# Optimization experiments

Hardware: AMD Instinct MI355X
Metric: run time of the kernel (lower is better)

## Reference

```python
import jax, jax.numpy as jnp
import numpy as np

B, LI, LJ, D = 32, 512, 512, 512
NN_DIM = 256  # agg output dim = 2*NN_DIM = 512


def setup_inputs() -> dict:
    key = jax.random.key(0)
    k1, k2, k3 = jax.random.split(key, 3)
    i = jax.random.normal(k1, (B, LI, D), dtype=jnp.float32)
    j = jax.random.normal(k2, (B, LJ, D), dtype=jnp.float32)
    W_agg = jax.random.normal(k3, (D, 2 * NN_DIM), dtype=jnp.float32) * (1.0 / np.sqrt(D))
    b_agg = jnp.zeros((2 * NN_DIM,), dtype=jnp.float32)
    return {"i": i, "j": j, "W_agg": W_agg, "b_agg": b_agg}


def _agg(x, W, b):
    # shared aggregation net: Dense(2*nn_dim) + tanh, then mean-pool over time
    # x: [B, L, D] -> [B, 2*nn_dim]
    return jnp.mean(jnp.tanh(jnp.einsum('bld,dh->blh', x, W) + b), axis=1)


def reference(i, j, W_agg, b_agg):
    # cross-attention scores: [B, Li, Lj]
    weight = jnp.einsum('bik,bjk->bij', i, j)
    # row softmax (over Lj) -> weights to aggregate j per i-position
    weight_j = jax.nn.softmax(weight, axis=2)
    # column softmax (over Li) -> weights to aggregate i per j-position
    weight_i = jax.nn.softmax(weight, axis=1)
    weighted_i = jnp.einsum('bij,bid->bjd', weight_i, i)  # [B, Lj, D]
    weighted_j = jnp.einsum('bij,bjd->bid', weight_j, j)  # [B, Li, D]
    output_i = jnp.abs(i - weighted_j)  # [B, Li, D]
    output_j = jnp.abs(j - weighted_i)  # [B, Lj, D]
    oi = _agg(output_i, W_agg, b_agg)   # [B, 2*nn_dim]
    oj = _agg(output_j, W_agg, b_agg)   # [B, 2*nn_dim]
    # K.mean(K.stack([oi, oj], axis=1), axis=1)
    return 0.5 * (oi + oj)
```

## Files before the change

kernel.cpp:

```cpp
#include <hip/hip_runtime.h>
#include <math.h>

#define B_ 32
#define L_ 512
#define D_ 512
#define H_ 512

typedef unsigned short u16;
typedef _Float16 h16;
typedef h16 half8 __attribute__((ext_vector_type(8)));
typedef float f32x4 __attribute__((ext_vector_type(4)));

#define SW(r, c) ((c) ^ (((r) >> 1) & 3))

typedef __attribute__((address_space(1))) void gvoid;
typedef __attribute__((address_space(3))) void svoid;
__device__ __forceinline__ void async_cp16(const void* g, void* l) {
    __builtin_amdgcn_global_load_lds((gvoid*)g, (svoid*)l, 16, 0, 0);
}

__device__ __forceinline__ u16 f2h(float x) {
    h16 h = (h16)x;
    u16 r;
    __builtin_memcpy(&r, &h, 2);
    return r;
}
__device__ __forceinline__ float h2f(u16 u) {
    h16 h;
    __builtin_memcpy(&h, &u, 2);
    return (float)h;
}
__device__ __forceinline__ float fast_tanh(float x) {
    return 1.0f - 2.0f / (__expf(2.0f * x) + 1.0f);
}

__device__ __forceinline__ void xcd_decode16(int n, int& z, int& tile) {
    int xcd = n & 7, w = n >> 3;
    z = xcd + 8 * (w >> 4);
    tile = w & 15;
}

__global__ __launch_bounds__(256) void cvt_all(const float* __restrict__ I,
                                               const float* __restrict__ Jm,
                                               const float* __restrict__ W,
                                               u16* __restrict__ Ih, u16* __restrict__ IhT,
                                               u16* __restrict__ Jh, u16* __restrict__ JhT,
                                               u16* __restrict__ WT,
                                               float* __restrict__ out) {
    const int z = blockIdx.z;
    const float* src;
    u16* h;
    u16* hT;
    size_t base;
    if (z < 32) {
        src = I; h = Ih; hT = IhT; base = (size_t)z * 512 * 512;
    } else if (z < 64) {
        src = Jm; h = Jh; hT = JhT; base = (size_t)(z - 32) * 512 * 512;
    } else {
        src = W; h = nullptr; hT = WT; base = 0;
        out[(blockIdx.y * 8 + blockIdx.x) * 256 + threadIdx.x] = 0.0f;
    }
    const int r0 = blockIdx.y * 64, c0 = blockIdx.x * 64;
    __shared__ u16 t[64][66];
    const int tid = threadIdx.x;
    const int tr = tid >> 4, tc4 = (tid & 15) * 4;
#pragma unroll
    for (int rep = 0; rep < 4; ++rep) {
        int r = rep * 16 + tr;
        f32x4 v = *(const f32x4*)(src + base + (size_t)(r0 + r) * 512 + c0 + tc4);
        unsigned h0 = f2h(v[0]), h1 = f2h(v[1]), h2 = f2h(v[2]), h3 = f2h(v[3]);
        if (h)
            *(uint2*)(h + base + (size_t)(r0 + r) * 512 + c0 + tc4) =
                make_uint2(h0 | (h1 << 16), h2 | (h3 << 16));
        t[r][tc4] = (u16)h0; t[r][tc4 + 1] = (u16)h1;
        t[r][tc4 + 2] = (u16)h2; t[r][tc4 + 3] = (u16)h3;
    }
    __syncthreads();
#pragma unroll
    for (int rep = 0; rep < 4; ++rep) {
        int r = rep * 16 + tr;
        unsigned a = t[tc4][r], b = t[tc4 + 1][r], c = t[tc4 + 2][r], d = t[tc4 + 3][r];
        *(uint2*)(hT + base + (size_t)(c0 + r) * 512 + r0 + tc4) =
            make_uint2(a | (b << 16), c | (d << 16));
    }
}

__global__ __launch_bounds__(256, 2) void score_mfma(const u16* __restrict__ Ih,
                                                     const u16* __restrict__ Jh,
                                                     u16* __restrict__ P_un,
                                                     u16* __restrict__ P_unT,
                                                     float* __restrict__ rtmax,
                                                     float* __restrict__ rtsum,
                                                     float* __restrict__ ctmax,
                                                     float* __restrict__ ctsum) {
    int b, tile;
    xcd_decode16(blockIdx.x, b, tile);
    const int i0 = (tile >> 2) * 128, j0 = (tile & 3) * 128;
    __shared__ u16 Ah[128 * 32], Bh[128 * 32];
    const int tid = threadIdx.x;
    const int wave = tid >> 6, lane = tid & 63;
    const int wm = (wave >> 1) * 64, wn = (wave & 1) * 64;
    const int lr = lane & 15, q = lane >> 4;
    const size_t boff = (size_t)b * L_ * D_;
    const u16* Ibh = Ih + boff;
    const u16* Jbh = Jh + boff;

    f32x4 acc[4][4] = {};

    for (int k0 = 0; k0 < D_; k0 += 32) {
#pragma unroll
        for (int h = 0; h < 2; ++h) {
            int g = wave * 2 + h;
            int r = g * 16 + (lane >> 2);
            int cg = SW(r, lane & 3);
            async_cp16(Ibh + (size_t)(i0 + r) * D_ + k0 + cg * 8, (char*)Ah + g * 1024);
            async_cp16(Jbh + (size_t)(j0 + r) * D_ + k0 + cg * 8, (char*)Bh + g * 1024);
        }
        __syncthreads();
        half8 af[4], bf[4];
#pragma unroll
        for (int mi = 0; mi < 4; ++mi) {
            int r = wm + mi * 16 + lr;
            af[mi] = *(const half8*)&Ah[r * 32 + SW(r, q) * 8];
        }
#pragma unroll
        for (int ni = 0; ni < 4; ++ni) {
            int r = wn + ni * 16 + lr;
            bf[ni] = *(const half8*)&Bh[r * 32 + SW(r, q) * 8];
        }
#pragma unroll
        for (int mi = 0; mi < 4; ++mi)
#pragma unroll
            for (int ni = 0; ni < 4; ++ni)
                acc[mi][ni] = __builtin_amdgcn_mfma_f32_16x16x32_f16(af[mi], bf[ni], acc[mi][ni], 0, 0, 0);
        __syncthreads();
    }

    float rm[4][4];
#pragma unroll
    for (int mi = 0; mi < 4; ++mi)
#pragma unroll
        for (int r4 = 0; r4 < 4; ++r4) {
            float t = fmaxf(fmaxf(acc[mi][0][r4], acc[mi][1][r4]),
                            fmaxf(acc[mi][2][r4], acc[mi][3][r4]));
#pragma unroll
            for (int off = 1; off < 16; off <<= 1) t = fmaxf(t, __shfl_xor(t, off));
            rm[mi][r4] = t;
        }
    float cm[4];
#pragma unroll
    for (int ni = 0; ni < 4; ++ni) {
        float u = -1e30f;
#pragma unroll
        for (int mi = 0; mi < 4; ++mi)
#pragma unroll
            for (int r4 = 0; r4 < 4; ++r4) u = fmaxf(u, acc[mi][ni][r4]);
        u = fmaxf(u, __shfl_xor(u, 16));
        u = fmaxf(u, __shfl_xor(u, 32));
        cm[ni] = u;
    }

    u16* Pu_b = P_un + (size_t)b * L_ * L_;
    u16* PuT_b = P_unT + (size_t)b * L_ * L_;
    float rs[4][4] = {};
    float cs[4] = {};
#pragma unroll
    for (int mi = 0; mi < 4; ++mi)
#pragma unroll
        for (int ni = 0; ni < 4; ++ni) {
            int i_base = i0 + wm + mi * 16 + q * 4;
            int j = j0 + wn + ni * 16 + lr;
            unsigned pc[4];
#pragma unroll
            for (int r4 = 0; r4 < 4; ++r4) {
                float er = __expf(acc[mi][ni][r4] - rm[mi][r4]);
                rs[mi][r4] += er;
                Pu_b[(size_t)(i_base + r4) * L_ + j] = f2h(er);
                float ec = __expf(acc[mi][ni][r4] - cm[ni]);
                cs[ni] += ec;
                pc[r4] = f2h(ec);
            }
            *(uint2*)&PuT_b[(size_t)j * L_ + i_base] =
                make_uint2(pc[0] | (pc[1] << 16), pc[2] | (pc[3] << 16));
        }

    const int gr = (j0 + wn) >> 6;
    const int gc = (i0 + wm) >> 6;
#pragma unroll
    for (int mi = 0; mi < 4; ++mi)
#pragma unroll
        for (int r4 = 0; r4 < 4; ++r4) {
            float s = rs[mi][r4];
#pragma unroll
            for (int off = 1; off < 16; off <<= 1) s += __shfl_xor(s, off);
            if (lr == 0) {
                int i = i0 + wm + mi * 16 + q * 4 + r4;
                rtmax[((size_t)b * L_ + i) * 8 + gr] = rm[mi][r4];
                rtsum[((size_t)b * L_ + i) * 8 + gr] = s;
            }
        }
#pragma unroll
    for (int ni = 0; ni < 4; ++ni) {
        float s = cs[ni];
        s += __shfl_xor(s, 16);
        s += __shfl_xor(s, 32);
        if (q == 0) {
            int j = j0 + wn + ni * 16 + lr;
            ctmax[((size_t)b * L_ + j) * 8 + gc] = cm[ni];
            ctsum[((size_t)b * L_ + j) * 8 + gc] = s;
        }
    }
}

__global__ __launch_bounds__(256, 2) void absdiff_scaled(const u16* __restrict__ P_un,
                                                         const u16* __restrict__ P_unT,
                                                         const float* __restrict__ rtmax,
                                                         const float* __restrict__ rtsum,
                                                         const float* __restrict__ ctmax,
                                                         const float* __restrict__ ctsum,
                                                         const u16* __restrict__ JhT,
                                                         const u16* __restrict__ IhT,
                                                         const u16* __restrict__ Ih,
                                                         const u16* __restrict__ Jh,
                                                         u16* __restrict__ Xall) {
    int zz, tile;
    xcd_decode16(blockIdx.x, zz, tile);
    const int side = zz >> 5, b = zz & 31;
    const int a0 = (tile >> 2) * 128, d0 = (tile & 3) * 128;
    const u16* Pb = (side ? P_unT : P_un) + (size_t)b * L_ * L_;
    const float* tmax = (side ? ctmax : rtmax) + (size_t)b * L_ * 8;
    const float* tsum = (side ? ctsum : rtsum) + (size_t)b * L_ * 8;
    const u16* Vt = (side ? IhT : JhT) + (size_t)b * D_ * L_;
    const u16* Oh = (side ? Jh : Ih) + (size_t)b * L_ * D_;
    u16* Xb = Xall + (size_t)zz * L_ * D_;

    __shared__ u16 As[128 * 32], Bs[128 * 32];
    __shared__ float sc[8][128];
    const int tid = threadIdx.x;
    const int wave = tid >> 6, lane = tid & 63;
    const int wm = (wave >> 1) * 64, wn = (wave & 1) * 64;
    const int lr = lane & 15, q = lane >> 4;

    if (tid < 128) {
        const float* tm = tmax + (size_t)(a0 + tid) * 8;
        const float* ts = tsum + (size_t)(a0 + tid) * 8;
        f32x4 m0 = *(const f32x4*)tm, m1 = *(const f32x4*)(tm + 4);
        f32x4 s0 = *(const f32x4*)ts, s1 = *(const f32x4*)(ts + 4);
        float m = fmaxf(fmaxf(fmaxf(m0[0], m0[1]), fmaxf(m0[2], m0[3])),
                        fmaxf(fmaxf(m1[0], m1[1]), fmaxf(m1[2], m1[3])));
        float e0 = __expf(m0[0] - m), e1 = __expf(m0[1] - m);
        float e2 = __expf(m0[2] - m), e3 = __expf(m0[3] - m);
        float e4 = __expf(m1[0] - m), e5 = __expf(m1[1] - m);
        float e6 = __expf(m1[2] - m), e7 = __expf(m1[3] - m);
        float inv = 1.0f / (e0 * s0[0] + e1 * s0[1] + e2 * s0[2] + e3 * s0[3] +
                            e4 * s1[0] + e5 * s1[1] + e6 * s1[2] + e7 * s1[3]);
        sc[0][tid] = e0 * inv; sc[1][tid] = e1 * inv;
        sc[2][tid] = e2 * inv; sc[3][tid] = e3 * inv;
        sc[4][tid] = e4 * inv; sc[5][tid] = e5 * inv;
        sc[6][tid] = e6 * inv; sc[7][tid] = e7 * inv;
    }
    __syncthreads();

    f32x4 acc[4][4] = {};

    for (int k0 = 0; k0 < L_; k0 += 32) {
#pragma unroll
        for (int h = 0; h < 2; ++h) {
            int g = wave * 2 + h;
            int r = g * 16 + (lane >> 2);
            int cg = SW(r, lane & 3);
            async_cp16(Pb + (size_t)(a0 + r) * L_ + k0 + cg * 8, (char*)As + g * 1024);
            async_cp16(Vt + (size_t)(d0 + r) * L_ + k0 + cg * 8, (char*)Bs + g * 1024);
        }
        __syncthreads();
        const int gk = k0 >> 6;
        half8 af[4], bf[4];
#pragma unroll
        for (int mi = 0; mi < 4; ++mi) {
            int r = wm + mi * 16 + lr;
            h16 s = (h16)sc[gk][r];
            half8 s8 = {s, s, s, s, s, s, s, s};
            af[mi] = *(const half8*)&As[r * 32 + SW(r, q) * 8] * s8;
        }
#pragma unroll
        for (int ni = 0; ni < 4; ++ni) {
            int r = wn + ni * 16 + lr;
            bf[ni] = *(const half8*)&Bs[r * 32 + SW(r, q) * 8];
        }
#pragma unroll
        for (int mi = 0; mi < 4; ++mi)
#pragma unroll
            for (int ni = 0; ni < 4; ++ni)
                acc[mi][ni] = __builtin_amdgcn_mfma_f32_16x16x32_f16(af[mi], bf[ni], acc[mi][ni], 0, 0, 0);
        __syncthreads();
    }

#pragma unroll
    for (int mi = 0; mi < 4; ++mi)
#pragma unroll
        for (int ni = 0; ni < 4; ++ni) {
            int i = a0 + wm + mi * 16 + q * 4;
            int d = d0 + wn + ni * 16 + lr;
#pragma unroll
            for (int r4 = 0; r4 < 4; ++r4) {
                float x = fabsf(h2f(Oh[(size_t)(i + r4) * D_ + d]) - acc[mi][ni][r4]);
                Xb[(size_t)(i + r4) * D_ + d] = f2h(x);
            }
        }
}

__global__ __launch_bounds__(512, 2) void agg_8ph(const u16* __restrict__ Xall,
                                                  const u16* __restrict__ Wt,
                                                  const float* __restrict__ bias,
                                                  float* __restrict__ out) {
    const int bid = blockIdx.x;
    const int n = bid >> 3;
    const int zz = (bid & 7) + 8 * (n >> 2);
    const int tile = n & 3;
    const int bb = zz & 31;
    const int l0 = (tile >> 1) * 256, h0 = (tile & 1) * 256;
    const u16* Xb = Xall + (size_t)zz * L_ * D_ + (size_t)l0 * D_;
    const u16* Wb = Wt + (size_t)h0 * D_;

    __shared__ u16 AL[2][2][8192];
    __shared__ u16 BL[2][2][8192];

    const int tid = threadIdx.x;
    const int wave = tid >> 6, lane = tid & 63;
    const int lr = lane & 15, q = lane >> 4;
    const int wr = wave >> 2, wc4 = wave & 3;

    const int ch0 = wave * 2;
    const int phys = lane * 16;
    const int Lb = phys ^ (((phys >> 6) & 3) << 4);
    const int sr = Lb >> 6;
    const int sk = (Lb & 63) >> 1;

#define ST_A(t, kh)                                                                     \
    do {                                                                                \
        char* dst_ = (char*)&AL[(t) & 1][(kh)][0];                                      \
        const u16* s_ = Xb + (t) * 64 + (kh) * 32 + sk;                                 \
        async_cp16(s_ + (size_t)(ch0 * 16 + sr) * D_, dst_ + ch0 * 1024);               \
        async_cp16(s_ + (size_t)(ch0 * 16 + 16 + sr) * D_, dst_ + ch0 * 1024 + 1024);   \
    } while (0)
#define ST_B(t, kh)                                                                     \
    do {                                                                                \
        char* dst_ = (char*)&BL[(t) & 1][(kh)][0];                                      \
        const u16* s_ = Wb + (t) * 64 + (kh) * 32 + sk;                                 \
        async_cp16(s_ + (size_t)(ch0 * 16 + sr) * D_, dst_ + ch0 * 1024);               \
        async_cp16(s_ + (size_t)(ch0 * 16 + 16 + sr) * D_, dst_ + ch0 * 1024 + 1024);   \
    } while (0)

    f32x4 acc[8][4] = {};

#define PHASE(t, mh, kk, STAGE_STMT, WAIT_STMT)                                         \
    do {                                                                                \
        const char* Ah_ = (const char*)&AL[(t) & 1][(kk)][0];                           \
        const char* Bh_ = (const char*)&BL[(t) & 1][(kk)][0];                           \
        half8 a_[4], b_[4];                                                             \
        _Pragma("unroll") for (int mi = 0; mi < 4; ++mi) {                              \
            int r_ = wr * 128 + (mh)*64 + mi * 16 + lr;                                 \
            a_[mi] = *(const half8*)(Ah_ + r_ * 64 + ((q * 16) ^ ((r_ & 3) << 4)));     \
        }                                                                               \
        _Pragma("unroll") for (int ni = 0; ni < 4; ++ni) {                              \
            int r_ = wc4 * 64 + ni * 16 + lr;                                           \
            b_[ni] = *(const half8*)(Bh_ + r_ * 64 + ((q * 16) ^ ((r_ & 3) << 4)));     \
        }                                                                               \
        STAGE_STMT;                                                                     \
        asm volatile("" ::: "memory");                                                  \
        __builtin_amdgcn_s_barrier();                                                   \
        asm volatile("" ::: "memory");                                                  \
        __builtin_amdgcn_s_setprio(1);                                                  \
        _Pragma("unroll") for (int mi = 0; mi < 4; ++mi)                                \
            _Pragma("unroll") for (int ni = 0; ni < 4; ++ni)                            \
                acc[(mh)*4 + mi][ni] = __builtin_amdgcn_mfma_f32_16x16x32_f16(          \
                    a_[mi], b_[ni], acc[(mh)*4 + mi][ni], 0, 0, 0);                     \
        __builtin_amdgcn_s_setprio(0);                                                  \
        WAIT_STMT;                                                                      \
        asm volatile("" ::: "memory");                                                  \
        __builtin_amdgcn_s_barrier();                                                   \
        asm volatile("" ::: "memory");                                                  \
    } while (0)

#define VM4 asm volatile("s_waitcnt vmcnt(4)" ::: "memory")
#define VM0 asm volatile("s_waitcnt vmcnt(0)" ::: "memory")

    ST_A(0, 0); ST_B(0, 0); ST_A(0, 1); ST_B(0, 1);
    ST_A(1, 0); ST_B(1, 0);
    VM4;
    asm volatile("" ::: "memory");
    __builtin_amdgcn_s_barrier();
    asm volatile("" ::: "memory");

    for (int it = 0; it < 4; ++it) {
        const int T = 2 * it, U = T + 1;
        const bool lastit = (it == 3);
        PHASE(T, 0, 0, { ST_A(U, 1); }, {});
        PHASE(T, 1, 0, { ST_B(U, 1); }, {});
        PHASE(T, 0, 1, { if (!lastit) ST_A(T + 2, 0); }, {});
        PHASE(T, 1, 1, { if (!lastit) ST_B(T + 2, 0); }, { if (lastit) VM0; else VM4; });
        PHASE(U, 0, 0, { if (!lastit) ST_A(T + 2, 1); }, {});
        PHASE(U, 1, 0, { if (!lastit) ST_B(T + 2, 1); }, {});
        PHASE(U, 0, 1, { if (!lastit) ST_A(T + 3, 0); }, {});
        PHASE(U, 1, 1, { if (!lastit) ST_B(T + 3, 0); }, { if (!lastit) VM4; });
    }

#pragma unroll
    for (int ni = 0; ni < 4; ++ni) {
        const int h = h0 + wc4 * 64 + ni * 16 + lr;
        const float bsv = bias[h];
        float ssum = 0.f;
#pragma unroll
        for (int mI = 0; mI < 8; ++mI)
#pragma unroll
            for (int r4 = 0; r4 < 4; ++r4)
                ssum += fast_tanh(acc[mI][ni][r4] + bsv);
        ssum += __shfl_xor(ssum, 16);
        ssum += __shfl_xor(ssum, 32);
        if (q == 0) atomicAdd(&out[bb * H_ + h], ssum * (0.5f / (float)L_));
    }
#undef PHASE
#undef ST_A
#undef ST_B
#undef VM4
#undef VM0
}

extern "C" void kernel_launch(void* const* d_in, const int* in_sizes, int n_in,
                              void* d_out, int out_size, void* d_ws, size_t ws_size,
                              hipStream_t stream) {
    const float* I = (const float*)d_in[0];
    const float* Jm = (const float*)d_in[1];
    const float* W = (const float*)d_in[2];
    const float* bias = (const float*)d_in[3];
    float* out = (float*)d_out;

    const size_t BLD = (size_t)B_ * L_ * D_;
    const size_t BLL = (size_t)B_ * L_ * L_;

    char* p = (char*)d_ws;
    auto give = [&](size_t bytes) {
        char* r = p;
        p += (bytes + 255) & ~(size_t)255;
        return r;
    };
    u16* Ih = (u16*)give(BLD * 2);
    u16* Jh = (u16*)give(BLD * 2);
    u16* IhT = (u16*)give(BLD * 2);
    u16* JhT = (u16*)give(BLD * 2);
    u16* WT = (u16*)give((size_t)D_ * H_ * 2);
    u16* P_un = (u16*)give(BLL * 2);
    u16* P_unT = (u16*)give(BLL * 2);
    float* rtmax = (float*)give((size_t)B_ * L_ * 8 * 4);
    float* rtsum = (float*)give((size_t)B_ * L_ * 8 * 4);
    float* ctmax = (float*)give((size_t)B_ * L_ * 8 * 4);
    float* ctsum = (float*)give((size_t)B_ * L_ * 8 * 4);
    u16* Xall = (u16*)give(2 * BLD * 2);

    cvt_all<<<dim3(8, 8, 65), 256, 0, stream>>>(I, Jm, W, Ih, IhT, Jh, JhT, WT, out);
    score_mfma<<<512, 256, 0, stream>>>(Ih, Jh, P_un, P_unT, rtmax, rtsum, ctmax, ctsum);
    absdiff_scaled<<<1024, 256, 0, stream>>>(P_un, P_unT, rtmax, rtsum, ctmax, ctsum,
                                             JhT, IhT, Ih, Jh, Xall);
    agg_8ph<<<256, 512, 0, stream>>>(Xall, WT, bias, out);
}
```

Measured before the change: 195.7 us.

## Rewrite absdiff GEMM as 256x256-tile eight-phase pipelined kernel with double-buffered async loads

Result: no change. 194.8 us (-0.4%).

```diff
diff --git a/kernel.cpp b/kernel.cpp
--- a/kernel.cpp
+++ b/kernel.cpp
@@ -212,38 +212,39 @@
     }
 }
 
-__global__ __launch_bounds__(256, 2) void absdiff_scaled(const u16* __restrict__ P_un,
-                                                         const u16* __restrict__ P_unT,
-                                                         const float* __restrict__ rtmax,
-                                                         const float* __restrict__ rtsum,
-                                                         const float* __restrict__ ctmax,
-                                                         const float* __restrict__ ctsum,
-                                                         const u16* __restrict__ JhT,
-                                                         const u16* __restrict__ IhT,
-                                                         const u16* __restrict__ Ih,
-                                                         const u16* __restrict__ Jh,
-                                                         u16* __restrict__ Xall) {
-    int zz, tile;
-    xcd_decode16(blockIdx.x, zz, tile);
+__global__ __launch_bounds__(512, 2) void absdiff_8ph(
+    const u16* __restrict__ P_un, const u16* __restrict__ P_unT,
+    const float* __restrict__ rtmax, const float* __restrict__ rtsum,
+    const float* __restrict__ ctmax, const float* __restrict__ ctsum,
+    const u16* __restrict__ JhT, const u16* __restrict__ IhT,
+    const u16* __restrict__ Ih, const u16* __restrict__ Jh,
+    u16* __restrict__ Xall) {
+    const int bid = blockIdx.x;
+    const int n = bid >> 3;
+    const int zz = (bid & 7) + 8 * (n >> 2);
+    const int tile = n & 3;
     const int side = zz >> 5, b = zz & 31;
-    const int a0 = (tile >> 2) * 128, d0 = (tile & 3) * 128;
-    const u16* Pb = (side ? P_unT : P_un) + (size_t)b * L_ * L_;
+    const int l0 = (tile >> 1) * 256, d0 = (tile & 1) * 256;
+
+    const u16* Pb = (side ? P_unT : P_un) + (size_t)b * L_ * L_ + (size_t)l0 * L_;
     const float* tmax = (side ? ctmax : rtmax) + (size_t)b * L_ * 8;
     const float* tsum = (side ? ctsum : rtsum) + (size_t)b * L_ * 8;
-    const u16* Vt = (side ? IhT : JhT) + (size_t)b * D_ * L_;
+    const u16* Vtb = (side ? IhT : JhT) + (size_t)b * (size_t)D_ * L_ + (size_t)d0 * L_;
     const u16* Oh = (side ? Jh : Ih) + (size_t)b * L_ * D_;
     u16* Xb = Xall + (size_t)zz * L_ * D_;
 
-    __shared__ u16 As[128 * 32], Bs[128 * 32];
-    __shared__ float sc[8][128];
+    __shared__ u16 AL[2][2][8192];
+    __shared__ u16 BL[2][2][8192];
+    __shared__ float scl[8][256];
+
     const int tid = threadIdx.x;
     const int wave = tid >> 6, lane = tid & 63;
-    const int wm = (wave >> 1) * 64, wn = (wave & 1) * 64;
     const int lr = lane & 15, q = lane >> 4;
-
-    if (tid < 128) {
-        const float* tm = tmax + (size_t)(a0 + tid) * 8;
-        const float* ts = tsum + (size_t)(a0 + tid) * 8;
+    const int wr = wave >> 2, wc4 = wave & 3;
+
+    if (tid < 256) {
+        const float* tm = tmax + (size_t)(l0 + tid) * 8;
+        const float* ts = tsum + (size_t)(l0 + tid) * 8;
         f32x4 m0 = *(const f32x4*)tm, m1 = *(const f32x4*)(tm + 4);
         f32x4 s0 = *(const f32x4*)ts, s1 = *(const f32x4*)(ts + 4);
         float m = fmaxf(fmaxf(fmaxf(m0[0], m0[1]), fmaxf(m0[2], m0[3])),
@@ -254,59 +255,111 @@
         float e6 = __expf(m1[2] - m), e7 = __expf(m1[3] - m);
         float inv = 1.0f / (e0 * s0[0] + e1 * s0[1] + e2 * s0[2] + e3 * s0[3] +
                             e4 * s1[0] + e5 * s1[1] + e6 * s1[2] + e7 * s1[3]);
-        sc[0][tid] = e0 * inv; sc[1][tid] = e1 * inv;
-        sc[2][tid] = e2 * inv; sc[3][tid] = e3 * inv;
-        sc[4][tid] = e4 * inv; sc[5][tid] = e5 * inv;
-        sc[6][tid] = e6 * inv; sc[7][tid] = e7 * inv;
-    }
-    __syncthreads();
-
-    f32x4 acc[4][4] = {};
-
-    for (int k0 = 0; k0 < L_; k0 += 32) {
-#pragma unroll
-        for (int h = 0; h < 2; ++h) {
-            int g = wave * 2 + h;
-            int r = g * 16 + (lane >> 2);
-            int cg = SW(r, lane & 3);
-            async_cp16(Pb + (size_t)(a0 + r) * L_ + k0 + cg * 8, (char*)As + g * 1024);
-            async_cp16(Vt + (size_t)(d0 + r) * L_ + k0 + cg * 8, (char*)Bs + g * 1024);
-        }
-        __syncthreads();
-        const int gk = k0 >> 6;
-        half8 af[4], bf[4];
-#pragma unroll
-        for (int mi = 0; mi < 4; ++mi) {
-            int r = wm + mi * 16 + lr;
-            h16 s = (h16)sc[gk][r];
-            half8 s8 = {s, s, s, s, s, s, s, s};
-            af[mi] = *(const half8*)&As[r * 32 + SW(r, q) * 8] * s8;
-        }
-#pragma unroll
-        for (int ni = 0; ni < 4; ++ni) {
-            int r = wn + ni * 16 + lr;
-            bf[ni] = *(const half8*)&Bs[r * 32 + SW(r, q) * 8];
-        }
+        scl[0][tid] = e0 * inv; scl[1][tid] = e1 * inv;
+        scl[2][tid] = e2 * inv; scl[3][tid] = e3 * inv;
+        scl[4][tid] = e4 * inv; scl[5][tid] = e5 * inv;
+        scl[6][tid] = e6 * inv; scl[7][tid] = e7 * inv;
+    }
+
+    const int ch0 = wave * 2;
+    const int phys = lane * 16;
+    const int Lb = phys ^ (((phys >> 6) & 3) << 4);
+    const int sr = Lb >> 6;
+    const int sk = (Lb & 63) >> 1;
+
+#define ST_A(t, kh)                                                                     \
+    do {                                                                                \
+        char* dst_ = (char*)&AL[(t) & 1][(kh)][0];                                      \
+        const u16* s_ = Pb + (t) * 64 + (kh) * 32 + sk;                                 \
+        async_cp16(s_ + (size_t)(ch0 * 16 + sr) * L_, dst_ + ch0 * 1024);               \
+        async_cp16(s_ + (size_t)(ch0 * 16 + 16 + sr) * L_, dst_ + ch0 * 1024 + 1024);   \
+    } while (0)
+#define ST_B(t, kh)                                                                     \
+    do {                                                                                \
+        char* dst_ = (char*)&BL[(t) & 1][(kh)][0];                                      \
+        const u16* s_ = Vtb + (t) * 64 + (kh) * 32 + sk;                                \
+        async_cp16(s_ + (size_t)(ch0 * 16 + sr) * L_, dst_ + ch0 * 1024);               \
+        async_cp16(s_ + (size_t)(ch0 * 16 + 16 + sr) * L_, dst_ + ch0 * 1024 + 1024);   \
+    } while (0)
+
+    f32x4 acc[8][4] = {};
+
+#define PHASE(t, mh, kk, STAGE_STMT, WAIT_STMT)                                         \
+    do {                                                                                \
+        const char* Ah_ = (const char*)&AL[(t) & 1][(kk)][0];                           \
+        const char* Bh_ = (const char*)&BL[(t) & 1][(kk)][0];                           \
+        half8 a_[4], b_[4];                                                             \
+        _Pragma("unroll") for (int mi = 0; mi < 4; ++mi) {                              \
+            int r_ = wr * 128 + (mh)*64 + mi * 16 + lr;                                 \
+            half8 av_ = *(const half8*)(Ah_ + r_ * 64 + ((q * 16) ^ ((r_ & 3) << 4)));  \
+            h16 s_ = (h16)scl[(t)][r_];                                                 \
+            half8 s8_ = {s_, s_, s_, s_, s_, s_, s_, s_};                               \
+            a_[mi] = av_ * s8_;                                                         \
+        }                                                                               \
+        _Pragma("unroll") for (int ni = 0; ni < 4; ++ni) {                              \
+            int r_ = wc4 * 64 + ni * 16 + lr;                                           \
+            b_[ni] = *(const half8*)(Bh_ + r_ * 64 + ((q * 16) ^ ((r_ & 3) << 4)));     \
+        }                                                                               \
+        STAGE_STMT;                                                                     \
+        asm volatile("" ::: "memory");                                                  \
+        __builtin_amdgcn_s_barrier();                                                   \
+        asm volatile("" ::: "memory");                                                  \
+        __builtin_amdgcn_s_setprio(1);                                                  \
+        _Pragma("unroll") for (int mi = 0; mi < 4; ++mi)                                \
+            _Pragma("unroll") for (int ni = 0; ni < 4; ++ni)                            \
+                acc[(mh)*4 + mi][ni] = __builtin_amdgcn_mfma_f32_16x16x32_f16(          \
+                    a_[mi], b_[ni], acc[(mh)*4 + mi][ni], 0, 0, 0);                     \
+        __builtin_amdgcn_s_setprio(0);                                                  \
+        WAIT_STMT;                                                                      \
+        asm volatile("" ::: "memory");                                                  \
+        __builtin_amdgcn_s_barrier();                                                   \
+        asm volatile("" ::: "memory");                                                  \
+    } while (0)
+
+#define VM4 asm volatile("s_waitcnt vmcnt(4)" ::: "memory")
+#define VM0 asm volatile("s_waitcnt vmcnt(0)" ::: "memory")
+
+    ST_A(0, 0); ST_B(0, 0); ST_A(0, 1); ST_B(0, 1);
+    ST_A(1, 0); ST_B(1, 0);
+    asm volatile("s_waitcnt lgkmcnt(0)" ::: "memory");
+    VM4;
+    asm volatile("" ::: "memory");
+    __builtin_amdgcn_s_barrier();
+    asm volatile("" ::: "memory");
+
+    for (int it = 0; it < 4; ++it) {
+        const int T = 2 * it, U = T + 1;
+        const bool lastit = (it == 3);
+        PHASE(T, 0, 0, { ST_A(U, 1); }, {});
+        PHASE(T, 1, 0, { ST_B(U, 1); }, {});
+        PHASE(T, 0, 1, { if (!lastit) ST_A(T + 2, 0); }, {});
+        PHASE(T, 1, 1, { if (!lastit) ST_B(T + 2, 0); }, { if (lastit) VM0; else VM4; });
+        PHASE(U, 0, 0, { if (!lastit) ST_A(T + 2, 1); }, {});
+        PHASE(U, 1, 0, { if (!lastit) ST_B(T + 2, 1); }, {});
+        PHASE(U, 0, 1, { if (!lastit) ST_A(T + 3, 0); }, {});
+        PHASE(U, 1, 1, { if (!lastit) ST_B(T + 3, 0); }, { if (!lastit) VM4; });
+    }
+
+#pragma unroll
+    for (int mh = 0; mh < 2; ++mh)
 #pragma unroll
         for (int mi = 0; mi < 4; ++mi)
 #pragma unroll
-            for (int ni = 0; ni < 4; ++ni)
-                acc[mi][ni] = __builtin_amdgcn_mfma_f32_16x16x32_f16(af[mi], bf[ni], acc[mi][ni], 0, 0, 0);
-        __syncthreads();
-    }
-
-#pragma unroll
-    for (int mi = 0; mi < 4; ++mi)
-#pragma unroll
-        for (int ni = 0; ni < 4; ++ni) {
-            int i = a0 + wm + mi * 16 + q * 4;
-            int d = d0 + wn + ni * 16 + lr;
-#pragma unroll
-            for (int r4 = 0; r4 < 4; ++r4) {
-                float x = fabsf(h2f(Oh[(size_t)(i + r4) * D_ + d]) - acc[mi][ni][r4]);
-                Xb[(size_t)(i + r4) * D_ + d] = f2h(x);
+            for (int ni = 0; ni < 4; ++ni) {
+                const int l_base = l0 + wr * 128 + mh * 64 + mi * 16 + q * 4;
+                const int d = d0 + wc4 * 64 + ni * 16 + lr;
+#pragma unroll
+                for (int r4 = 0; r4 < 4; ++r4) {
+                    float x = fabsf(h2f(Oh[(size_t)(l_base + r4) * D_ + d]) -
+                                    acc[mh * 4 + mi][ni][r4]);
+                    Xb[(size_t)(l_base + r4) * D_ + d] = f2h(x);
+                }
             }
-        }
+#undef PHASE
+#undef ST_A
+#undef ST_B
+#undef VM4
+#undef VM0
 }
 
 __global__ __launch_bounds__(512, 2) void agg_8ph(const u16* __restrict__ Xall,
@@ -459,7 +512,7 @@
 
     cvt_all<<<dim3(8, 8, 65), 256, 0, stream>>>(I, Jm, W, Ih, IhT, Jh, JhT, WT, out);
     score_mfma<<<512, 256, 0, stream>>>(Ih, Jh, P_un, P_unT, rtmax, rtsum, ctmax, ctsum);
-    absdiff_scaled<<<1024, 256, 0, stream>>>(P_un, P_unT, rtmax, rtsum, ctmax, ctsum,
-                                             JhT, IhT, Ih, Jh, Xall);
+    absdiff_8ph<<<256, 512, 0, stream>>>(P_un, P_unT, rtmax, rtsum, ctmax, ctsum,
+                                         JhT, IhT, Ih, Jh, Xall);
     agg_8ph<<<256, 512, 0, stream>>>(Xall, WT, bias, out);
 }
```
